# Kernel optimization log

Measured on AMD Instinct MI355X. Metric: run time of the kernel, lower is better.

The kernel has to match this reference:

```python
import jax, jax.numpy as jnp
import numpy as np

LN_EPS = 1e-5  # nn.LayerNorm default
N_HEAD = 12


def layer_norm(x, w, b, eps=LN_EPS):
    m = jnp.mean(x, axis=-1, keepdims=True)
    v = jnp.var(x, axis=-1, keepdims=True)
    return (x - m) * jax.lax.rsqrt(v + eps) * w + b


def mha(x, in_proj_w, in_proj_b, out_w, out_b, n_head):
    # x: [B,S,D]; self-attention, q=k=v=x (torch nn.MultiheadAttention math)
    B, S, D = x.shape
    hd = D // n_head
    qkv = x @ in_proj_w.T + in_proj_b              # [B,S,3D]
    q, k, v = jnp.split(qkv, 3, axis=-1)
    q = q.reshape(B, S, n_head, hd)
    k = k.reshape(B, S, n_head, hd)
    v = v.reshape(B, S, n_head, hd)
    scale = 1.0 / jnp.sqrt(jnp.asarray(hd, x.dtype))
    scores = jnp.einsum('bqhd,bkhd->bhqk', q, k) * scale  # [B,H,S,S]
    attn = jax.nn.softmax(scores, axis=-1)
    o = jnp.einsum('bhqk,bkhd->bqhd', attn, v).reshape(B, S, D)
    return o @ out_w.T + out_b


def setup_inputs() -> dict:
    key = jax.random.key(0)
    ks = jax.random.split(key, 8)
    B, S, D = 4, 2048, 768
    d_ff = 4 * D
    sd = 0.02
    return {
        'x': jax.random.normal(ks[0], (B, S, D), jnp.float32),
        'ln1_w': jnp.ones((D,), jnp.float32),
        'ln1_b': jnp.zeros((D,), jnp.float32),
        'in_proj_w': jax.random.normal(ks[1], (3 * D, D), jnp.float32) * sd,
        'in_proj_b': jax.random.normal(ks[2], (3 * D,), jnp.float32) * sd,
        'out_w': jax.random.normal(ks[3], (D, D), jnp.float32) * sd,
        'out_b': jax.random.normal(ks[4], (D,), jnp.float32) * sd,
        'ln2_w': jnp.ones((D,), jnp.float32),
        'ln2_b': jnp.zeros((D,), jnp.float32),
        'fc_w': jax.random.normal(ks[5], (d_ff, D), jnp.float32) * sd,
        'fc_b': jnp.zeros((d_ff,), jnp.float32),
        'proj_w': jax.random.normal(ks[6], (D, d_ff), jnp.float32) * sd,
        'proj_b': jnp.zeros((D,), jnp.float32),
    }


def reference(x, ln1_w, ln1_b, in_proj_w, in_proj_b, out_w, out_b,
              ln2_w, ln2_b, fc_w, fc_b, proj_w, proj_b):
    h = layer_norm(x, ln1_w, ln1_b)
    x = x + mha(h, in_proj_w, in_proj_b, out_w, out_b, N_HEAD)
    h2 = layer_norm(x, ln2_w, ln2_b)
    mlp = jax.nn.gelu(h2 @ fc_w.T + fc_b, approximate=False) @ proj_w.T + proj_b
    return x + mlp
```

## Files before the change

### kernel.cpp

```cpp
#include <hip/hip_runtime.h>
#include <hip/hip_bf16.h>
#include <math.h>

#define D_MODEL 768
#define N_HEADS 12
#define HD 64
#define SEQ 2048
#define BATCH 4
#define M_ROWS 8192
#define D_FF 3072
#define QKV_DIM 2304
#define LN_EPS 1e-5f
#define Q_SCALE 0.18033688011112042f

typedef __attribute__((ext_vector_type(8))) short bf16x8;
typedef __attribute__((ext_vector_type(4))) float f32x4;
typedef __hip_bfloat16 bf16;

__device__ __forceinline__ void store_val(float* p, float v) { *p = v; }
__device__ __forceinline__ void store_val(bf16* p, float v) { *p = __float2bfloat16(v); }

__device__ __forceinline__ unsigned int pack_bf16_pair(float a, float b) {
    unsigned int ua = __builtin_bit_cast(unsigned int, a) + 0x8000u;
    unsigned int ub = __builtin_bit_cast(unsigned int, b) + 0x8000u;
    return __builtin_amdgcn_perm(ub, ua, 0x07060302u);
}

__device__ __forceinline__ void async_load16(const void* g, void* l) {
    __builtin_amdgcn_global_load_lds(
        (const __attribute__((address_space(1))) void*)g,
        (__attribute__((address_space(3))) void*)l, 16, 0, 0);
}

__global__ __launch_bounds__(256) void ln1_cast(
        const float* __restrict__ x, const float* __restrict__ w,
        const float* __restrict__ b, bf16* __restrict__ y,
        const float* __restrict__ s0, bf16* __restrict__ d0, int n0,
        const float* __restrict__ s1, bf16* __restrict__ d1, int n1,
        const float* __restrict__ s2, bf16* __restrict__ d2, int n2,
        const float* __restrict__ s3, bf16* __restrict__ d3, int n3) {
    int t = threadIdx.x;
    if (blockIdx.x >= M_ROWS) {
        int i = (blockIdx.x - M_ROWS) * 256 + t;
        const float* s; bf16* d; int local = i;
        if (local < n0) { s = s0; d = d0; }
        else {
            local -= n0;
            if (local < n1) { s = s1; d = d1; }
            else {
                local -= n1;
                if (local < n2) { s = s2; d = d2; }
                else {
                    local -= n2;
                    if (local >= n3) return;
                    s = s3; d = d3;
                }
            }
        }
        float4 v = ((const float4*)s)[local];
        uint2 pk;
        pk.x = pack_bf16_pair(v.x, v.y);
        pk.y = pack_bf16_pair(v.z, v.w);
        *(uint2*)(d + local * 4) = pk;
        return;
    }
    int row = blockIdx.x;
    const float* xr = x + (size_t)row * D_MODEL;
    bf16* yr = y + (size_t)row * D_MODEL;
    float v0 = xr[t], v1 = xr[t + 256], v2 = xr[t + 512];
    float s  = v0 + v1 + v2;
    float sq = v0 * v0 + v1 * v1 + v2 * v2;
    #pragma unroll
    for (int off = 32; off; off >>= 1) {
        s  += __shfl_xor(s, off);
        sq += __shfl_xor(sq, off);
    }
    __shared__ float ss[4], ssq[4];
    int wave = t >> 6;
    if ((t & 63) == 0) { ss[wave] = s; ssq[wave] = sq; }
    __syncthreads();
    s  = ss[0] + ss[1] + ss[2] + ss[3];
    sq = ssq[0] + ssq[1] + ssq[2] + ssq[3];
    float mean = s * (1.0f / D_MODEL);
    float var  = sq * (1.0f / D_MODEL) - mean * mean;
    float rstd = rsqrtf(var + LN_EPS);
    yr[t]       = __float2bfloat16((v0 - mean) * rstd * w[t]       + b[t]);
    yr[t + 256] = __float2bfloat16((v1 - mean) * rstd * w[t + 256] + b[t + 256]);
    yr[t + 512] = __float2bfloat16((v2 - mean) * rstd * w[t + 512] + b[t + 512]);
}

template <typename OutT>
__global__ __launch_bounds__(256) void ln_kernel(const float* __restrict__ x,
                                                 const float* __restrict__ w,
                                                 const float* __restrict__ b,
                                                 OutT* __restrict__ y) {
    int row = blockIdx.x;
    const float* xr = x + (size_t)row * D_MODEL;
    OutT* yr = y + (size_t)row * D_MODEL;
    int t = threadIdx.x;
    float v0 = xr[t], v1 = xr[t + 256], v2 = xr[t + 512];
    float s  = v0 + v1 + v2;
    float sq = v0 * v0 + v1 * v1 + v2 * v2;
    #pragma unroll
    for (int off = 32; off; off >>= 1) {
        s  += __shfl_xor(s, off);
        sq += __shfl_xor(sq, off);
    }
    __shared__ float ss[4], ssq[4];
    int wave = t >> 6;
    if ((t & 63) == 0) { ss[wave] = s; ssq[wave] = sq; }
    __syncthreads();
    s  = ss[0] + ss[1] + ss[2] + ss[3];
    sq = ssq[0] + ssq[1] + ssq[2] + ssq[3];
    float mean = s * (1.0f / D_MODEL);
    float var  = sq * (1.0f / D_MODEL) - mean * mean;
    float rstd = rsqrtf(var + LN_EPS);
    store_val(yr + t,       (v0 - mean) * rstd * w[t]       + b[t]);
    store_val(yr + t + 256, (v1 - mean) * rstd * w[t + 256] + b[t + 256]);
    store_val(yr + t + 512, (v2 - mean) * rstd * w[t + 512] + b[t + 512]);
}

__device__ __forceinline__ float gelu_fast(float v) {
    float u = v * (0.7978845608f + 0.0356774081f * v * v);
    u = fminf(fmaxf(u, -10.0f), 10.0f);
    float e = __builtin_amdgcn_exp2f(u * 2.8853900818f);
    float th = (e - 1.0f) * __builtin_amdgcn_rcpf(e + 1.0f);
    return 0.5f * v * (1.0f + th);
}

template <int FUSE, typename OutT>
__global__ __launch_bounds__(256) void gemm_mfma(const bf16* __restrict__ A,
                                                 const bf16* __restrict__ W,
                                                 const float* __restrict__ bias,
                                                 const float* __restrict__ resid,
                                                 OutT* __restrict__ C,
                                                 int M, int N, int K) {
    const int BK = 64;
    __shared__ __align__(16) bf16 As[128 * BK];
    __shared__ __align__(16) bf16 Bs[128 * BK];
    int t = threadIdx.x;
    int wave = t >> 6, lane = t & 63;
    int m_base = blockIdx.y * 128, n_base = blockIdx.x * 128;
    int wm = (wave >> 1) * 64, wn = (wave & 1) * 64;
    int c = lane & 15, rr = lane >> 4;

    f32x4 acc[4][4] = {};

    const bf16* Ag[4]; const bf16* Bg[4];
    bf16* Al[4]; bf16* Bl[4];
    #pragma unroll
    for (int r = 0; r < 4; r++) {
        int s = r * 256 + t;
        int row = s >> 3, p = s & 7;
        int kc = p ^ (row & 7);
        Ag[r] = A + (size_t)(m_base + row) * K + kc * 8;
        Bg[r] = W + (size_t)(n_base + row) * K + kc * 8;
        Al[r] = As + (r * 256 + wave * 64) * 8;
        Bl[r] = Bs + (r * 256 + wave * 64) * 8;
    }

    for (int k0 = 0; k0 < K; k0 += BK) {
        __syncthreads();
        #pragma unroll
        for (int r = 0; r < 4; r++) {
            async_load16(Ag[r] + k0, Al[r]);
            async_load16(Bg[r] + k0, Bl[r]);
        }
        __syncthreads();

        #pragma unroll
        for (int kk = 0; kk < 2; kk++) {
            int sw = ((kk * 4 + rr) ^ (c & 7)) * 8;
            bf16x8 af[4], bfr[4];
            #pragma unroll
            for (int mi = 0; mi < 4; mi++)
                af[mi] = *(const bf16x8*)&As[(wm + mi * 16 + c) * BK + sw];
            #pragma unroll
            for (int ni = 0; ni < 4; ni++)
                bfr[ni] = *(const bf16x8*)&Bs[(wn + ni * 16 + c) * BK + sw];
            #pragma unroll
            for (int mi = 0; mi < 4; mi++)
                #pragma unroll
                for (int ni = 0; ni < 4; ni++)
                    acc[mi][ni] = __builtin_amdgcn_mfma_f32_16x16x32_bf16(
                        bfr[ni], af[mi], acc[mi][ni], 0, 0, 0);
        }
    }

    #pragma unroll
    for (int mi = 0; mi < 4; mi++) {
        int m = m_base + wm + mi * 16 + c;
        #pragma unroll
        for (int ni = 0; ni < 4; ni++) {
            int n0 = n_base + wn + ni * 16 + rr * 4;
            float4 bv = *(const float4*)&bias[n0];
            float v0 = acc[mi][ni][0] + bv.x;
            float v1 = acc[mi][ni][1] + bv.y;
            float v2 = acc[mi][ni][2] + bv.z;
            float v3 = acc[mi][ni][3] + bv.w;
            if (FUSE == 1) {
                v0 = gelu_fast(v0); v1 = gelu_fast(v1);
                v2 = gelu_fast(v2); v3 = gelu_fast(v3);
            }
            if (FUSE == 2) {
                float4 rv = *(const float4*)&resid[(size_t)m * N + n0];
                v0 += rv.x; v1 += rv.y; v2 += rv.z; v3 += rv.w;
            }
            if (FUSE == 3 && n0 < 768) {
                v0 *= Q_SCALE; v1 *= Q_SCALE; v2 *= Q_SCALE; v3 *= Q_SCALE;
            }
            OutT* dst = C + (size_t)m * N + n0;
            if (sizeof(OutT) == 4) {
                float4 st = {v0, v1, v2, v3};
                *(float4*)dst = st;
            } else {
                uint2 pk;
                pk.x = pack_bf16_pair(v0, v1);
                pk.y = pack_bf16_pair(v2, v3);
                *(uint2*)dst = pk;
            }
        }
    }
}

__global__ __launch_bounds__(256) void vtrans(const bf16* __restrict__ qkvb,
                                              bf16* __restrict__ vt) {
    __shared__ bf16 T[64 * 72];
    int t = threadIdx.x;
    int s0 = blockIdx.x * 64, h = blockIdx.y, b = blockIdx.z;
    const bf16* src = qkvb + (size_t)(b * SEQ) * QKV_DIM + 2 * D_MODEL + h * HD;
    #pragma unroll
    for (int i = 0; i < 2; i++) {
        int idx = i * 256 + t;
        int sr = idx >> 3, ch = idx & 7;
        uint4 v = *(const uint4*)(src + (size_t)(s0 + sr) * QKV_DIM + ch * 8);
        *(uint4*)&T[sr * 72 + ch * 8] = v;
    }
    __syncthreads();
    int dr = t >> 2, part = t & 3;
    unsigned int w[8];
    #pragma unroll
    for (int i = 0; i < 8; i++) {
        unsigned short a, bsh;
        __builtin_memcpy(&a,   &T[(part * 16 + 2 * i    ) * 72 + dr], 2);
        __builtin_memcpy(&bsh, &T[(part * 16 + 2 * i + 1) * 72 + dr], 2);
        w[i] = (unsigned int)a | ((unsigned int)bsh << 16);
    }
    bf16* dst = vt + ((size_t)((b * N_HEADS + h) * HD + dr)) * SEQ + s0 + part * 16;
    uint4 p0; p0.x = w[0]; p0.y = w[1]; p0.z = w[2]; p0.w = w[3];
    uint4 p1; p1.x = w[4]; p1.y = w[5]; p1.z = w[6]; p1.w = w[7];
    *(uint4*)dst = p0;
    *(uint4*)(dst + 8) = p1;
}

__global__ __launch_bounds__(256) void attn_mfma(const bf16* __restrict__ qkvb,
                                                 const bf16* __restrict__ vt,
                                                 bf16* __restrict__ o) {
    __shared__ __align__(16) bf16 Ks[2 * 64 * 64];
    __shared__ __align__(16) bf16 Vts[2 * 64 * 64];
    __shared__ __align__(16) bf16 Ps[128 * 64];

    int t = threadIdx.x;
    int wave = t >> 6, lane = t & 63;
    int qt = blockIdx.x, h = blockIdx.y, b = blockIdx.z;
    int s0 = qt * 128;
    int wq = wave * 32;
    int c = lane & 15, rr = lane >> 4;
    int cx = c & 7;

    const bf16* qbase  = qkvb + (size_t)b * SEQ * QKV_DIM + h * HD;
    const bf16* kbase  = qbase + D_MODEL;
    const bf16* vtbase = vt + (size_t)((b * N_HEADS + h) * HD) * SEQ;

    int srow = t >> 3, sp = t & 7;
    int skc = sp ^ (srow & 7);

    #pragma unroll
    for (int r = 0; r < 4; r++) {
        int lin = r * 256 + t;
        int qq = lin >> 3, p = lin & 7;
        int kc = p ^ (qq & 7);
        async_load16(qbase + (size_t)(s0 + qq) * QKV_DIM + kc * 8,
                     Ps + (size_t)(r * 256 + wave * 64) * 8);
    }
    #pragma unroll
    for (int r = 0; r < 2; r++) {
        int row = (r * 256 + t) >> 3;
        int kc = ((r * 256 + t) & 7) ^ (row & 7);
        async_load16(kbase + (size_t)row * QKV_DIM + kc * 8,
                     Ks + (size_t)(r * 256 + wave * 64) * 8);
        async_load16(vtbase + (size_t)row * SEQ + kc * 8,
                     Vts + (size_t)(r * 256 + wave * 64) * 8);
    }
    __syncthreads();

    bf16x8 bq[2][2];
    #pragma unroll
    for (int m = 0; m < 2; m++)
        #pragma unroll
        for (int kk = 0; kk < 2; kk++)
            bq[m][kk] = *(const bf16x8*)&Ps[(wq + m * 16 + c) * 64 + ((kk * 4 + rr) ^ cx) * 8];

    bf16x8 ones;
    #pragma unroll
    for (int i = 0; i < 8; i++) ones[i] = (short)0x3F80;

    f32x4 Oa[2][4] = {};
    f32x4 La[2] = {};

    for (int jt = 0; jt < SEQ; jt += 64) {
        int cur = (jt >> 6) & 1;
        bf16* Kb  = Ks  + cur * 4096;
        bf16* Vtb = Vts + cur * 4096;

        if (jt + 64 < SEQ) {
            bf16* Kn  = Ks  + (cur ^ 1) * 4096;
            bf16* Vtn = Vts + (cur ^ 1) * 4096;
            #pragma unroll
            for (int r = 0; r < 2; r++) {
                int row = (r * 256 + t) >> 3;
                int kc = ((r * 256 + t) & 7) ^ (row & 7);
                async_load16(kbase + (size_t)(jt + 64 + row) * QKV_DIM + kc * 8,
                             Kn + (size_t)(r * 256 + wave * 64) * 8);
                async_load16(vtbase + (size_t)row * SEQ + (jt + 64) + kc * 8,
                             Vtn + (size_t)(r * 256 + wave * 64) * 8);
            }
        }

        f32x4 St[4][2] = {};
        __builtin_amdgcn_s_setprio(1);
        #pragma unroll
        for (int kk = 0; kk < 2; kk++) {
            bf16x8 ak[4];
            #pragma unroll
            for (int jj = 0; jj < 4; jj++)
                ak[jj] = *(const bf16x8*)&Kb[(jj * 16 + c) * 64 + ((kk * 4 + rr) ^ cx) * 8];
            #pragma unroll
            for (int jj = 0; jj < 4; jj++)
                #pragma unroll
                for (int m = 0; m < 2; m++)
                    St[jj][m] = __builtin_amdgcn_mfma_f32_16x16x32_bf16(
                        ak[jj], bq[m][kk], St[jj][m], 0, 0, 0);
        }
        __builtin_amdgcn_s_setprio(0);

        #pragma unroll
        for (int jj = 0; jj < 4; jj++) {
            int off = ((jj * 2 + (rr >> 1)) ^ cx) * 8 + (rr & 1) * 4;
            #pragma unroll
            for (int m = 0; m < 2; m++) {
                float p0 = __builtin_amdgcn_exp2f(St[jj][m][0]);
                float p1 = __builtin_amdgcn_exp2f(St[jj][m][1]);
                float p2 = __builtin_amdgcn_exp2f(St[jj][m][2]);
                float p3 = __builtin_amdgcn_exp2f(St[jj][m][3]);
                uint2 pk;
                pk.x = pack_bf16_pair(p0, p1);
                pk.y = pack_bf16_pair(p2, p3);
                *(uint2*)&Ps[(wq + m * 16 + c) * 64 + off] = pk;
            }
        }

        __builtin_amdgcn_s_setprio(1);
        #pragma unroll
        for (int kk = 0; kk < 2; kk++) {
            bf16x8 ap[2];
            #pragma unroll
            for (int m = 0; m < 2; m++)
                ap[m] = *(const bf16x8*)&Ps[(wq + m * 16 + c) * 64 + ((kk * 4 + rr) ^ cx) * 8];
            #pragma unroll
            for (int m = 0; m < 2; m++)
                La[m] = __builtin_amdgcn_mfma_f32_16x16x32_bf16(
                    ap[m], ones, La[m], 0, 0, 0);
            #pragma unroll
            for (int n = 0; n < 4; n++) {
                bf16x8 bv = *(const bf16x8*)&Vtb[(n * 16 + c) * 64 + ((kk * 4 + rr) ^ cx) * 8];
                #pragma unroll
                for (int m = 0; m < 2; m++)
                    Oa[m][n] = __builtin_amdgcn_mfma_f32_16x16x32_bf16(
                        ap[m], bv, Oa[m][n], 0, 0, 0);
            }
        }
        __builtin_amdgcn_s_setprio(0);

        __syncthreads();
    }

    #pragma unroll
    for (int m = 0; m < 2; m++)
        #pragma unroll
        for (int rg = 0; rg < 4; rg++) {
            float inv = __builtin_amdgcn_rcpf(La[m][rg]);
            int q = s0 + wq + m * 16 + rr * 4 + rg;
            bf16* op = o + (size_t)(b * SEQ + q) * D_MODEL + h * HD;
            #pragma unroll
            for (int n = 0; n < 4; n++)
                op[n * 16 + c] = __float2bfloat16(Oa[m][n][rg] * inv);
        }
}

extern "C" void kernel_launch(void* const* d_in, const int* in_sizes, int n_in,
                              void* d_out, int out_size, void* d_ws, size_t ws_size,
                              hipStream_t stream) {
    const float* x         = (const float*)d_in[0];
    const float* ln1_w     = (const float*)d_in[1];
    const float* ln1_b     = (const float*)d_in[2];
    const float* in_proj_w = (const float*)d_in[3];
    const float* in_proj_b = (const float*)d_in[4];
    const float* out_w     = (const float*)d_in[5];
    const float* out_b     = (const float*)d_in[6];
    const float* ln2_w     = (const float*)d_in[7];
    const float* ln2_b     = (const float*)d_in[8];
    const float* fc_w      = (const float*)d_in[9];
    const float* fc_b      = (const float*)d_in[10];
    const float* proj_w    = (const float*)d_in[11];
    const float* proj_b    = (const float*)d_in[12];

    float* out = (float*)d_out;
    char*  ws  = (char*)d_ws;

    bf16* qkvb = (bf16*)ws;
    bf16* vt   = (bf16*)(ws + 37748736);
    bf16* ff   = (bf16*)ws;
    bf16* h    = (bf16*)(ws + 50331648);
    bf16* o    = (bf16*)(ws + 62914560);
    bf16* wbf  = (bf16*)(ws + 75497472);
    bf16* wqkv_b  = wbf;
    bf16* wout_b  = wqkv_b + (size_t)QKV_DIM * D_MODEL;
    bf16* wfc_b   = wout_b + (size_t)D_MODEL * D_MODEL;
    bf16* wproj_b = wfc_b  + (size_t)D_FF * D_MODEL;

    int n0 = QKV_DIM * D_MODEL / 4, n1 = D_MODEL * D_MODEL / 4;
    int n2 = D_FF * D_MODEL / 4,    n3 = D_MODEL * D_FF / 4;
    int cast_blocks = (n0 + n1 + n2 + n3 + 255) / 256;

    ln1_cast<<<M_ROWS + cast_blocks, 256, 0, stream>>>(
        x, ln1_w, ln1_b, h,
        in_proj_w, wqkv_b, n0, out_w, wout_b, n1, fc_w, wfc_b, n2, proj_w, wproj_b, n3);
    gemm_mfma<3, bf16><<<dim3(QKV_DIM / 128, M_ROWS / 128), 256, 0, stream>>>(
        h, wqkv_b, in_proj_b, nullptr, qkvb, M_ROWS, QKV_DIM, D_MODEL);
    vtrans<<<dim3(SEQ / 64, N_HEADS, BATCH), 256, 0, stream>>>(qkvb, vt);
    attn_mfma<<<dim3(SEQ / 128, N_HEADS, BATCH), 256, 0, stream>>>(qkvb, vt, o);
    gemm_mfma<2, float><<<dim3(D_MODEL / 128, M_ROWS / 128), 256, 0, stream>>>(
        o, wout_b, out_b, x, out, M_ROWS, D_MODEL, D_MODEL);
    ln_kernel<bf16><<<M_ROWS, 256, 0, stream>>>(out, ln2_w, ln2_b, h);
    gemm_mfma<1, bf16><<<dim3(D_FF / 128, M_ROWS / 128), 256, 0, stream>>>(
        h, wfc_b, fc_b, nullptr, ff, M_ROWS, D_FF, D_MODEL);
    gemm_mfma<2, float><<<dim3(D_MODEL / 128, M_ROWS / 128), 256, 0, stream>>>(
        ff, wproj_b, proj_b, out, out, M_ROWS, D_MODEL, D_FF);
}
```

Measured before the change: 404.8 us.

## Double-buffer GEMM shared-memory tiles to overlap global loads with MFMA

```diff
diff --git a/kernel.cpp b/kernel.cpp
--- a/kernel.cpp
+++ b/kernel.cpp
@@ -136,8 +136,8 @@
                                                  OutT* __restrict__ C,
                                                  int M, int N, int K) {
     const int BK = 64;
-    __shared__ __align__(16) bf16 As[128 * BK];
-    __shared__ __align__(16) bf16 Bs[128 * BK];
+    __shared__ __align__(16) bf16 As[2][128 * BK];
+    __shared__ __align__(16) bf16 Bs[2][128 * BK];
     int t = threadIdx.x;
     int wave = t >> 6, lane = t & 63;
     int m_base = blockIdx.y * 128, n_base = blockIdx.x * 128;
@@ -147,7 +147,7 @@
     f32x4 acc[4][4] = {};
 
     const bf16* Ag[4]; const bf16* Bg[4];
-    bf16* Al[4]; bf16* Bl[4];
+    int loff[4];
     #pragma unroll
     for (int r = 0; r < 4; r++) {
         int s = r * 256 + t;
@@ -155,18 +155,27 @@
         int kc = p ^ (row & 7);
         Ag[r] = A + (size_t)(m_base + row) * K + kc * 8;
         Bg[r] = W + (size_t)(n_base + row) * K + kc * 8;
-        Al[r] = As + (r * 256 + wave * 64) * 8;
-        Bl[r] = Bs + (r * 256 + wave * 64) * 8;
-    }
-
-    for (int k0 = 0; k0 < K; k0 += BK) {
-        __syncthreads();
-        #pragma unroll
-        for (int r = 0; r < 4; r++) {
-            async_load16(Ag[r] + k0, Al[r]);
-            async_load16(Bg[r] + k0, Bl[r]);
-        }
-        __syncthreads();
+        loff[r] = (r * 256 + wave * 64) * 8;
+    }
+
+    #pragma unroll
+    for (int r = 0; r < 4; r++) {
+        async_load16(Ag[r], As[0] + loff[r]);
+        async_load16(Bg[r], Bs[0] + loff[r]);
+    }
+    __syncthreads();
+
+    int nk = K / BK;
+    for (int ki = 0; ki < nk; ki++) {
+        int cur = ki & 1;
+        if (ki + 1 < nk) {
+            int k0n = (ki + 1) * BK;
+            #pragma unroll
+            for (int r = 0; r < 4; r++) {
+                async_load16(Ag[r] + k0n, As[cur ^ 1] + loff[r]);
+                async_load16(Bg[r] + k0n, Bs[cur ^ 1] + loff[r]);
+            }
+        }
 
         #pragma unroll
         for (int kk = 0; kk < 2; kk++) {
@@ -174,10 +183,10 @@
             bf16x8 af[4], bfr[4];
             #pragma unroll
             for (int mi = 0; mi < 4; mi++)
-                af[mi] = *(const bf16x8*)&As[(wm + mi * 16 + c) * BK + sw];
+                af[mi] = *(const bf16x8*)&As[cur][(wm + mi * 16 + c) * BK + sw];
             #pragma unroll
             for (int ni = 0; ni < 4; ni++)
-                bfr[ni] = *(const bf16x8*)&Bs[(wn + ni * 16 + c) * BK + sw];
+                bfr[ni] = *(const bf16x8*)&Bs[cur][(wn + ni * 16 + c) * BK + sw];
             #pragma unroll
             for (int mi = 0; mi < 4; mi++)
                 #pragma unroll
@@ -185,6 +194,7 @@
                     acc[mi][ni] = __builtin_amdgcn_mfma_f32_16x16x32_bf16(
                         bfr[ni], af[mi], acc[mi][ni], 0, 0, 0);
         }
+        __syncthreads();
     }
 
     #pragma unroll
@@ -271,9 +281,6 @@
     const bf16* qbase  = qkvb + (size_t)b * SEQ * QKV_DIM + h * HD;
     const bf16* kbase  = qbase + D_MODEL;
     const bf16* vtbase = vt + (size_t)((b * N_HEADS + h) * HD) * SEQ;
-
-    int srow = t >> 3, sp = t & 7;
-    int skc = sp ^ (srow & 7);
 
     #pragma unroll
     for (int r = 0; r < 4; r++) {
```

Result: faster. 394.8 us (-2.5%).
